# Optimization experiments

Hardware: AMD Instinct MI355X
Metric: run time of the kernel (lower is better)

## Reference

```python
import jax, jax.numpy as jnp
import numpy as np

GAMMA = 0.99
LAM = 0.95
CLIP = 0.2
VALUE_COEFF = 0.5
ENTROPY_COEFF = 0.01
T = 500_000
S = 128
A = 16


def _mlp(x, W1, b1, W2, b2, W3, b3):
    h = jax.nn.relu(x @ W1 + b1)
    h = jax.nn.relu(h @ W2 + b2)
    return h @ W3 + b3


def setup_inputs() -> dict:
    key = jax.random.key(0)
    ks = jax.random.split(key, 12)
    states = jax.random.normal(ks[0], (T, S), dtype=jnp.float32)
    next_states = jax.random.normal(ks[1], (T, S), dtype=jnp.float32)
    rewards = jax.random.normal(ks[2], (T,), dtype=jnp.float32)
    dones = (jax.random.uniform(ks[3], (T,)) < 0.01).astype(jnp.float32)
    actions = jax.random.randint(ks[4], (T,), 0, A)
    # old log-probs of taken actions (valid log-probabilities)
    old_logp = jnp.log(jax.random.uniform(ks[5], (T,), minval=1e-3, maxval=1.0))

    def lin(k, fan_in, fan_out):
        lim = 1.0 / np.sqrt(fan_in)
        return jax.random.uniform(k, (fan_in, fan_out), minval=-lim, maxval=lim, dtype=jnp.float32)

    return {
        'states': states, 'next_states': next_states, 'rewards': rewards,
        'dones': dones, 'actions': actions, 'old_logp': old_logp,
        'aW1': lin(ks[6], S, 64), 'ab1': jnp.zeros((64,), jnp.float32),
        'aW2': lin(ks[7], 64, 64), 'ab2': jnp.zeros((64,), jnp.float32),
        'aW3': lin(ks[8], 64, A), 'ab3': jnp.zeros((A,), jnp.float32),
        'cW1': lin(ks[9], S, 64), 'cb1': jnp.zeros((64,), jnp.float32),
        'cW2': lin(ks[10], 64, 64), 'cb2': jnp.zeros((64,), jnp.float32),
        'cW3': lin(ks[11], 64, 1), 'cb3': jnp.zeros((1,), jnp.float32),
    }


def reference(states, next_states, rewards, dones, actions, old_logp,
              aW1, ab1, aW2, ab2, aW3, ab3,
              cW1, cb1, cW2, cb2, cW3, cb3):
    # ---- critic values and TD deltas ----
    values = _mlp(states, cW1, cb1, cW2, cb2, cW3, cb3)[:, 0]        # [T]
    next_values = _mlp(next_states, cW1, cb1, cW2, cb2, cW3, cb3)[:, 0]
    not_done = 1.0 - dones
    deltas = rewards + GAMMA * next_values * not_done - values       # [T]

    # ---- GAE: reverse-time linear recurrence a_t = c_t * a_{t+1} + d_t ----
    coef = GAMMA * LAM * not_done

    def step(carry, cd):
        c, d = cd
        a = c * carry + d
        return a, a

    _, advantages = jax.lax.scan(step, jnp.float32(0.0), (coef, deltas), reverse=True)
    returns = advantages + values
    adv_n = (advantages - advantages.mean()) / (jnp.std(advantages, ddof=1) + 1e-8)

    # ---- actor: clipped surrogate ----
    probs = jax.nn.softmax(_mlp(states, aW1, ab1, aW2, ab2, aW3, ab3), axis=-1)  # [T, A]
    logp = jnp.log(jnp.take_along_axis(probs, actions[:, None], axis=1))[:, 0]   # [T]
    ratios = jnp.exp(logp - old_logp)
    surr1 = ratios * adv_n
    surr2 = jnp.clip(ratios, 1.0 - CLIP, 1.0 + CLIP) * adv_n
    actor_loss = -jnp.minimum(surr1, surr2).mean()

    # ---- critic MSE loss ----
    critic_loss = jnp.mean((values - returns) ** 2)

    # ---- entropy bonus ----
    entropy_loss = jnp.mean(-jnp.sum(probs * jnp.log(probs + 1e-8), axis=-1))

    total_loss = actor_loss + VALUE_COEFF * critic_loss - ENTROPY_COEFF * entropy_loss
    return jnp.stack([total_loss, actor_loss, critic_loss, entropy_loss])
```

## Files before the change

kernel.cpp:

```cpp
#include <hip/hip_runtime.h>
#include <hip/hip_bf16.h>

#define T_N 500000
#define NTILE 31250
#define NBLK 512
#define NWAVES (NBLK * 4)
#define NCHUNK 4096
#define CHUNKL 128
#define NPART 1024

typedef __attribute__((ext_vector_type(8))) short short8v;
typedef __attribute__((ext_vector_type(4))) float float4v;

__device__ __forceinline__ short f2bf(float f) {
    __hip_bfloat16 b = __float2bfloat16(f);
    return *reinterpret_cast<short*>(&b);
}

__device__ __forceinline__ short8v cvt8(const float4 a, const float4 b) {
    short8v r;
    r[0] = f2bf(a.x); r[1] = f2bf(a.y); r[2] = f2bf(a.z); r[3] = f2bf(a.w);
    r[4] = f2bf(b.x); r[5] = f2bf(b.y); r[6] = f2bf(b.z); r[7] = f2bf(b.w);
    return r;
}

#define FC1 0
#define FA1 16
#define FC2 32
#define FA2 40
#define FA3 48
#define NFRAG 50

__global__ __launch_bounds__(64) void k_pack(
    const float* __restrict__ cW1, const float* __restrict__ aW1,
    const float* __restrict__ cW2, const float* __restrict__ aW2,
    const float* __restrict__ aW3, short8v* __restrict__ packed)
{
    const int f = blockIdx.x, l = threadIdx.x;
    const int g = l >> 4, col = l & 15;
    const float* W; int s, c, ncol;
    if (f < FA1)      { W = cW1; s = f >> 2;         c = f & 3;         ncol = 64; }
    else if (f < FC2) { W = aW1; s = (f - FA1) >> 2; c = (f - FA1) & 3; ncol = 64; }
    else if (f < FA2) { W = cW2; s = (f - FC2) >> 2; c = (f - FC2) & 3; ncol = 64; }
    else if (f < FA3) { W = aW2; s = (f - FA2) >> 2; c = (f - FA2) & 3; ncol = 64; }
    else              { W = aW3; s = f - FA3;        c = 0;             ncol = 16; }
    short8v frag;
    #pragma unroll
    for (int j = 0; j < 8; ++j) {
        int k = s * 32 + g * 8 + j;
        frag[j] = f2bf(W[k * ncol + c * 16 + col]);
    }
    packed[f * 64 + l] = frag;
}

__device__ __forceinline__ void store_h(short (*hb)[68], const float4v* acc, int g, int q) {
    #pragma unroll
    for (int c = 0; c < 4; ++c)
        #pragma unroll
        for (int r = 0; r < 4; ++r)
            hb[g * 4 + r][c * 16 + q] = f2bf(fmaxf(acc[c][r], 0.f));
}

__global__ __launch_bounds__(256) void k_mlp(
    const float* __restrict__ states, const float* __restrict__ next_states,
    const float* __restrict__ rewards, const float* __restrict__ dones,
    const int* __restrict__ actions, const float* __restrict__ old_logp,
    const short8v* __restrict__ pk,
    const float* __restrict__ cb1, const float* __restrict__ ab1,
    const float* __restrict__ cb2, const float* __restrict__ ab2,
    const float* __restrict__ ab3,
    const float* __restrict__ cW3, const float* __restrict__ cb3,
    float* __restrict__ delta_o, float* __restrict__ coef_o,
    float* __restrict__ ratio_o, float* __restrict__ ent_o)
{
    __shared__ __align__(16) short8v spk[NFRAG * 64];
    __shared__ __align__(16) short hlds[4][2][16][68];
    const int wv = threadIdx.x >> 6, l = threadIdx.x & 63;
    const int g = l >> 4, q = l & 15;
    short (*h0)[68] = hlds[wv][0];
    short (*h1)[68] = hlds[wv][1];

    for (int i = threadIdx.x; i < NFRAG * 64; i += 256) spk[i] = pk[i];
    __syncthreads();

    int tile = blockIdx.x * 4 + wv;
    if (tile >= NTILE) return;

    float bc1[4], bc2[4], ba1[4], ba2[4], w3[4];
    #pragma unroll
    for (int c = 0; c < 4; ++c) {
        bc1[c] = cb1[c * 16 + q];
        bc2[c] = cb2[c * 16 + q];
        ba1[c] = ab1[c * 16 + q];
        ba2[c] = ab2[c * 16 + q];
        w3[c]  = cW3[c * 16 + q];
    }
    const float ab3q = ab3[q];
    const float cb3v = cb3[0];

    float4 rs[8], rn[8];
    {
        const float* xs = states + ((long long)tile * 16 + q) * 128 + g * 8;
        const float* xn = next_states + ((long long)tile * 16 + q) * 128 + g * 8;
        #pragma unroll
        for (int s = 0; s < 4; ++s) {
            rs[2 * s]     = *reinterpret_cast<const float4*>(xs + s * 32);
            rs[2 * s + 1] = *reinterpret_cast<const float4*>(xs + s * 32 + 4);
            rn[2 * s]     = *reinterpret_cast<const float4*>(xn + s * 32);
            rn[2 * s + 1] = *reinterpret_cast<const float4*>(xn + s * 32 + 4);
        }
    }

    while (true) {
        const int next = tile + NWAVES;
        const long long r0 = (long long)tile * 16;

        short8v sa[4], na[4];
        #pragma unroll
        for (int s = 0; s < 4; ++s) {
            sa[s] = cvt8(rs[2 * s], rs[2 * s + 1]);
            na[s] = cvt8(rn[2 * s], rn[2 * s + 1]);
        }

        if (next < NTILE) {
            const float* xs = states + ((long long)next * 16 + q) * 128 + g * 8;
            const float* xn = next_states + ((long long)next * 16 + q) * 128 + g * 8;
            #pragma unroll
            for (int s = 0; s < 4; ++s) {
                rs[2 * s]     = *reinterpret_cast<const float4*>(xs + s * 32);
                rs[2 * s + 1] = *reinterpret_cast<const float4*>(xs + s * 32 + 4);
                rn[2 * s]     = *reinterpret_cast<const float4*>(xn + s * 32);
                rn[2 * s + 1] = *reinterpret_cast<const float4*>(xn + s * 32 + 4);
            }
        }

        float4v accC[4], accN[4];
        #pragma unroll
        for (int c = 0; c < 4; ++c) {
            accC[c] = (float4v){bc1[c], bc1[c], bc1[c], bc1[c]};
            accN[c] = accC[c];
        }
        #pragma unroll
        for (int s = 0; s < 4; ++s) {
            #pragma unroll
            for (int c = 0; c < 4; ++c) {
                short8v w = spk[(FC1 + s * 4 + c) * 64 + l];
                accC[c] = __builtin_amdgcn_mfma_f32_16x16x32_bf16(sa[s], w, accC[c], 0, 0, 0);
                accN[c] = __builtin_amdgcn_mfma_f32_16x16x32_bf16(na[s], w, accN[c], 0, 0, 0);
            }
        }
        store_h(h0, accC, g, q);
        store_h(h1, accN, g, q);

        float4v c2C[4], c2N[4];
        #pragma unroll
        for (int c = 0; c < 4; ++c) {
            c2C[c] = (float4v){bc2[c], bc2[c], bc2[c], bc2[c]};
            c2N[c] = c2C[c];
        }
        #pragma unroll
        for (int s = 0; s < 2; ++s) {
            short8v aC = *reinterpret_cast<const short8v*>(&h0[q][s * 32 + g * 8]);
            short8v aN = *reinterpret_cast<const short8v*>(&h1[q][s * 32 + g * 8]);
            #pragma unroll
            for (int c = 0; c < 4; ++c) {
                short8v w = spk[(FC2 + s * 4 + c) * 64 + l];
                c2C[c] = __builtin_amdgcn_mfma_f32_16x16x32_bf16(aC, w, c2C[c], 0, 0, 0);
                c2N[c] = __builtin_amdgcn_mfma_f32_16x16x32_bf16(aN, w, c2N[c], 0, 0, 0);
            }
        }
        float vr[4] = {0.f, 0.f, 0.f, 0.f}, nr[4] = {0.f, 0.f, 0.f, 0.f};
        #pragma unroll
        for (int c = 0; c < 4; ++c) {
            #pragma unroll
            for (int r = 0; r < 4; ++r) {
                vr[r] = fmaf(fmaxf(c2C[c][r], 0.f), w3[c], vr[r]);
                nr[r] = fmaf(fmaxf(c2N[c][r], 0.f), w3[c], nr[r]);
            }
        }
        #pragma unroll
        for (int o = 1; o < 16; o <<= 1)
            #pragma unroll
            for (int r = 0; r < 4; ++r) {
                vr[r] += __shfl_xor(vr[r], o);
                nr[r] += __shfl_xor(nr[r], o);
            }
        float v[4], nv[4];
        #pragma unroll
        for (int r = 0; r < 4; ++r) { v[r] = vr[r] + cb3v; nv[r] = nr[r] + cb3v; }

        float4v aA[4];
        #pragma unroll
        for (int c = 0; c < 4; ++c) aA[c] = (float4v){ba1[c], ba1[c], ba1[c], ba1[c]};
        #pragma unroll
        for (int s = 0; s < 4; ++s)
            #pragma unroll
            for (int c = 0; c < 4; ++c)
                aA[c] = __builtin_amdgcn_mfma_f32_16x16x32_bf16(sa[s], spk[(FA1 + s * 4 + c) * 64 + l], aA[c], 0, 0, 0);
        store_h(h0, aA, g, q);

        float4v a2[4];
        #pragma unroll
        for (int c = 0; c < 4; ++c) a2[c] = (float4v){ba2[c], ba2[c], ba2[c], ba2[c]};
        #pragma unroll
        for (int s = 0; s < 2; ++s) {
            short8v aa = *reinterpret_cast<const short8v*>(&h0[q][s * 32 + g * 8]);
            #pragma unroll
            for (int c = 0; c < 4; ++c)
                a2[c] = __builtin_amdgcn_mfma_f32_16x16x32_bf16(aa, spk[(FA2 + s * 4 + c) * 64 + l], a2[c], 0, 0, 0);
        }
        store_h(h1, a2, g, q);

        float4v a3 = (float4v){ab3q, ab3q, ab3q, ab3q};
        #pragma unroll
        for (int s = 0; s < 2; ++s) {
            short8v aa = *reinterpret_cast<const short8v*>(&h1[q][s * 32 + g * 8]);
            a3 = __builtin_amdgcn_mfma_f32_16x16x32_bf16(aa, spk[(FA3 + s) * 64 + l], a3, 0, 0, 0);
        }

        float lg[4], mx[4], pe[4], se[4], tt[4], ent[4], logp[4];
        #pragma unroll
        for (int r = 0; r < 4; ++r) { lg[r] = a3[r]; mx[r] = lg[r]; }
        #pragma unroll
        for (int o = 1; o < 16; o <<= 1)
            #pragma unroll
            for (int r = 0; r < 4; ++r) mx[r] = fmaxf(mx[r], __shfl_xor(mx[r], o));
        #pragma unroll
        for (int r = 0; r < 4; ++r) {
            pe[r] = __expf(lg[r] - mx[r]);
            se[r] = pe[r];
            tt[r] = pe[r] * lg[r];
        }
        #pragma unroll
        for (int o = 1; o < 16; o <<= 1)
            #pragma unroll
            for (int r = 0; r < 4; ++r) {
                se[r] += __shfl_xor(se[r], o);
                tt[r] += __shfl_xor(tt[r], o);
            }
        const int4 av = *reinterpret_cast<const int4*>(&actions[r0 + g * 4]);
        const int act[4] = {av.x, av.y, av.z, av.w};
        #pragma unroll
        for (int r = 0; r < 4; ++r) {
            float ls = __logf(se[r]);
            ent[r] = mx[r] + ls - tt[r] / se[r];
            float sel = __shfl(lg[r], (l & 48) | act[r]);
            logp[r] = sel - mx[r] - ls;
        }

        if (q == 0) {
            const long long rb = r0 + g * 4;
            const float4 rw = *reinterpret_cast<const float4*>(&rewards[rb]);
            const float4 dn = *reinterpret_cast<const float4*>(&dones[rb]);
            const float4 ol = *reinterpret_cast<const float4*>(&old_logp[rb]);
            const float rwv[4] = {rw.x, rw.y, rw.z, rw.w};
            const float dnv[4] = {dn.x, dn.y, dn.z, dn.w};
            const float olv[4] = {ol.x, ol.y, ol.z, ol.w};
            const float GL = 0.99f * 0.95f;
            float dl[4], cf[4], rt[4];
            #pragma unroll
            for (int r = 0; r < 4; ++r) {
                float nd = 1.f - dnv[r];
                dl[r] = fmaf(0.99f * nd, nv[r], rwv[r]) - v[r];
                cf[r] = GL * nd;
                rt[r] = __expf(logp[r] - olv[r]);
            }
            float4 t;
            t.x = dl[0]; t.y = dl[1]; t.z = dl[2]; t.w = dl[3];
            *reinterpret_cast<float4*>(&delta_o[rb]) = t;
            t.x = cf[0]; t.y = cf[1]; t.z = cf[2]; t.w = cf[3];
            *reinterpret_cast<float4*>(&coef_o[rb]) = t;
            t.x = rt[0]; t.y = rt[1]; t.z = rt[2]; t.w = rt[3];
            *reinterpret_cast<float4*>(&ratio_o[rb]) = t;
            t.x = ent[0]; t.y = ent[1]; t.z = ent[2]; t.w = ent[3];
            *reinterpret_cast<float4*>(&ent_o[rb]) = t;
        }

        if (next >= NTILE) break;
        tile = next;
    }
}

__global__ __launch_bounds__(256) void k_gae_chunk(
    const float* __restrict__ coef, const float* __restrict__ delta,
    float* __restrict__ P, float* __restrict__ Q)
{
    const int c = blockIdx.x * 256 + threadIdx.x;
    const long long lo = (long long)c * CHUNKL;
    float p = 1.f, a = 0.f;
    if (lo < T_N) {
        const int n = (int)((T_N - lo < CHUNKL) ? (T_N - lo) : CHUNKL);
        for (int j = (n >> 2) - 1; j >= 0; --j) {
            float4 cfv = *reinterpret_cast<const float4*>(&coef[lo + 4 * j]);
            float4 dlv = *reinterpret_cast<const float4*>(&delta[lo + 4 * j]);
            a = fmaf(cfv.w, a, dlv.w);
            a = fmaf(cfv.z, a, dlv.z);
            a = fmaf(cfv.y, a, dlv.y);
            a = fmaf(cfv.x, a, dlv.x);
            p *= cfv.x * cfv.y * cfv.z * cfv.w;
        }
    }
    P[c] = p; Q[c] = a;
}

__global__ __launch_bounds__(1024) void k_gae_scan(
    const float* __restrict__ P, const float* __restrict__ Q,
    float* __restrict__ carry)
{
    __shared__ float sp[1024], sq[1024];
    const int t = threadIdx.x, b = t * 4;
    float p = P[b + 3], q = Q[b + 3];
    #pragma unroll
    for (int c = 2; c >= 0; --c) {
        float pc = P[b + c], qc = Q[b + c];
        q = fmaf(pc, q, qc);
        p = pc * p;
    }
    sp[t] = p; sq[t] = q;
    __syncthreads();
    for (int d = 1; d < 1024; d <<= 1) {
        float pp = sp[t], qq = sq[t];
        float p2 = 1.f, q2 = 0.f;
        const bool has = (t + d) < 1024;
        if (has) { p2 = sp[t + d]; q2 = sq[t + d]; }
        __syncthreads();
        if (has) { sp[t] = pp * p2; sq[t] = fmaf(pp, q2, qq); }
        __syncthreads();
    }
    float x = (t + 1 < 1024) ? sq[t + 1] : 0.f;
    #pragma unroll
    for (int c = 3; c >= 0; --c) {
        carry[b + c] = x;
        x = fmaf(P[b + c], x, Q[b + c]);
    }
}

__global__ __launch_bounds__(256) void k_gae_apply(
    const float* __restrict__ coef, const float* __restrict__ delta,
    const float* __restrict__ carry, float* __restrict__ adv,
    float* __restrict__ part)
{
    const int c = blockIdx.x * 256 + threadIdx.x;
    const long long lo = (long long)c * CHUNKL;
    float s = 0.f, s2 = 0.f;
    if (lo < T_N) {
        const int n = (int)((T_N - lo < CHUNKL) ? (T_N - lo) : CHUNKL);
        float a = carry[c];
        for (int j = (n >> 2) - 1; j >= 0; --j) {
            float4 cfv = *reinterpret_cast<const float4*>(&coef[lo + 4 * j]);
            float4 dlv = *reinterpret_cast<const float4*>(&delta[lo + 4 * j]);
            float a3 = fmaf(cfv.w, a, dlv.w);
            float a2v = fmaf(cfv.z, a3, dlv.z);
            float a1 = fmaf(cfv.y, a2v, dlv.y);
            float a0 = fmaf(cfv.x, a1, dlv.x);
            float4 o; o.x = a0; o.y = a1; o.z = a2v; o.w = a3;
            *reinterpret_cast<float4*>(&adv[lo + 4 * j]) = o;
            a = a0;
            s += a0 + a1 + a2v + a3;
            s2 += a0 * a0 + a1 * a1 + a2v * a2v + a3 * a3;
        }
    }
    #pragma unroll
    for (int o = 32; o > 0; o >>= 1) { s += __shfl_down(s, o); s2 += __shfl_down(s2, o); }
    __shared__ float l0[4], l1[4];
    const int wv = threadIdx.x >> 6, ln = threadIdx.x & 63;
    if (ln == 0) { l0[wv] = s; l1[wv] = s2; }
    __syncthreads();
    if (threadIdx.x == 0) {
        part[blockIdx.x * 2]     = l0[0] + l0[1] + l0[2] + l0[3];
        part[blockIdx.x * 2 + 1] = l1[0] + l1[1] + l1[2] + l1[3];
    }
}

__global__ __launch_bounds__(256) void k_actor(
    const float* __restrict__ adv, const float* __restrict__ ratio,
    const float* __restrict__ ent, const float* __restrict__ part,
    float* __restrict__ part4)
{
    __shared__ float st[2];
    if (threadIdx.x == 0) {
        float S = 0.f, S2 = 0.f;
        #pragma unroll
        for (int i = 0; i < 16; ++i) { S += part[2 * i]; S2 += part[2 * i + 1]; }
        const float Tf = (float)T_N;
        float mean = S / Tf;
        float var = (S2 - S * S / Tf) / (Tf - 1.f);
        st[0] = mean;
        st[1] = 1.f / (sqrtf(fmaxf(var, 0.f)) + 1e-8f);
    }
    __syncthreads();
    const float mean = st[0], isd = st[1];
    float sm = 0.f, se = 0.f;
    for (long long i = (long long)blockIdx.x * 256 + threadIdx.x; i < T_N;
         i += (long long)gridDim.x * 256) {
        float an = (adv[i] - mean) * isd;
        float rt = ratio[i];
        float s1 = rt * an;
        float s2v = fminf(fmaxf(rt, 0.8f), 1.2f) * an;
        sm += fminf(s1, s2v);
        se += ent[i];
    }
    #pragma unroll
    for (int o = 32; o > 0; o >>= 1) { sm += __shfl_down(sm, o); se += __shfl_down(se, o); }
    __shared__ float l0[4], l1[4];
    const int wv = threadIdx.x >> 6, ln = threadIdx.x & 63;
    if (ln == 0) { l0[wv] = sm; l1[wv] = se; }
    __syncthreads();
    if (threadIdx.x == 0) {
        part4[blockIdx.x * 2]     = l0[0] + l0[1] + l0[2] + l0[3];
        part4[blockIdx.x * 2 + 1] = l1[0] + l1[1] + l1[2] + l1[3];
    }
}

__global__ __launch_bounds__(1024) void k_final(
    const float* __restrict__ part4, const float* __restrict__ part,
    float* __restrict__ out)
{
    const int t = threadIdx.x;
    float sm = part4[t * 2], se = part4[t * 2 + 1];
    #pragma unroll
    for (int o = 32; o > 0; o >>= 1) { sm += __shfl_down(sm, o); se += __shfl_down(se, o); }
    __shared__ float l0[16], l1[16];
    const int wv = t >> 6, ln = t & 63;
    if (ln == 0) { l0[wv] = sm; l1[wv] = se; }
    __syncthreads();
    if (t == 0) {
        float SM = 0.f, SE = 0.f;
        #pragma unroll
        for (int i = 0; i < 16; ++i) { SM += l0[i]; SE += l1[i]; }
        float S2 = 0.f;
        #pragma unroll
        for (int i = 0; i < 16; ++i) S2 += part[2 * i + 1];
        const float Tf = (float)T_N;
        float actor_loss = -SM / Tf;
        float ent_loss = SE / Tf;
        float critic_loss = S2 / Tf;
        float total = actor_loss + 0.5f * critic_loss - 0.01f * ent_loss;
        out[0] = total; out[1] = actor_loss; out[2] = critic_loss; out[3] = ent_loss;
    }
}

extern "C" void kernel_launch(void* const* d_in, const int* in_sizes, int n_in,
                              void* d_out, int out_size, void* d_ws, size_t ws_size,
                              hipStream_t stream) {
    (void)in_sizes; (void)n_in; (void)out_size; (void)ws_size;
    const float* states      = (const float*)d_in[0];
    const float* next_states = (const float*)d_in[1];
    const float* rewards     = (const float*)d_in[2];
    const float* dones       = (const float*)d_in[3];
    const int*   actions     = (const int*)d_in[4];
    const float* old_logp    = (const float*)d_in[5];
    const float* aW1 = (const float*)d_in[6];  const float* ab1 = (const float*)d_in[7];
    const float* aW2 = (const float*)d_in[8];  const float* ab2 = (const float*)d_in[9];
    const float* aW3 = (const float*)d_in[10]; const float* ab3 = (const float*)d_in[11];
    const float* cW1 = (const float*)d_in[12]; const float* cb1 = (const float*)d_in[13];
    const float* cW2 = (const float*)d_in[14]; const float* cb2 = (const float*)d_in[15];
    const float* cW3 = (const float*)d_in[16]; const float* cb3 = (const float*)d_in[17];
    float* out = (float*)d_out;

    float* ws = (float*)d_ws;
    float* delta = ws;
    float* coef  = ws + 1 * (size_t)T_N;
    float* ratio = ws + 2 * (size_t)T_N;
    float* entb  = ws + 3 * (size_t)T_N;
    float* adv   = ws + 4 * (size_t)T_N;
    float* P     = ws + 5 * (size_t)T_N;
    float* Q     = P + NCHUNK;
    float* carry = Q + NCHUNK;
    float* part  = carry + NCHUNK;
    float* part4 = part + 32;
    short8v* packed = (short8v*)(part4 + 2048);

    k_pack<<<NFRAG, 64, 0, stream>>>(cW1, aW1, cW2, aW2, aW3, packed);
    k_mlp<<<NBLK, 256, 0, stream>>>(
        states, next_states, rewards, dones, actions, old_logp, packed,
        cb1, ab1, cb2, ab2, ab3, cW3, cb3, delta, coef, ratio, entb);
    k_gae_chunk<<<NCHUNK / 256, 256, 0, stream>>>(coef, delta, P, Q);
    k_gae_scan<<<1, 1024, 0, stream>>>(P, Q, carry);
    k_gae_apply<<<NCHUNK / 256, 256, 0, stream>>>(coef, delta, carry, adv, part);
    k_actor<<<NPART, 256, 0, stream>>>(adv, ratio, entb, part, part4);
    k_final<<<1, 1024, 0, stream>>>(part4, part, out);
}
```

Before: 211.8 us.

## Move softmax epilogue from MLP kernel into actor reduction, store bf16 logits

The MLP kernel no longer does the per-row softmax, entropy, log-prob and delta/coef computation. It now writes only the critic values, next values and the 16 actor logits per row, the logits as bf16. The GAE kernels recompute delta and coef on the fly from values, rewards and dones, and the actor kernel recomputes the softmax, entropy and ratio from the stored logits. The aim is to cut shuffle-heavy epilogue work and extra input loads from the MLP kernel, which dominates the runtime. The cost is more intermediate memory traffic (a 32-byte logit row instead of a few floats), four input streams in each GAE pass, and some precision loss from rounding logits to bf16.

```diff
diff --git a/kernel.cpp b/kernel.cpp
--- a/kernel.cpp
+++ b/kernel.cpp
@@ -15,6 +15,9 @@
 __device__ __forceinline__ short f2bf(float f) {
     __hip_bfloat16 b = __float2bfloat16(f);
     return *reinterpret_cast<short*>(&b);
+}
+__device__ __forceinline__ float bf2f(short s) {
+    return __uint_as_float(((unsigned)(unsigned short)s) << 16);
 }
 
 __device__ __forceinline__ short8v cvt8(const float4 a, const float4 b) {
@@ -63,15 +66,13 @@
 
 __global__ __launch_bounds__(256) void k_mlp(
     const float* __restrict__ states, const float* __restrict__ next_states,
-    const float* __restrict__ rewards, const float* __restrict__ dones,
-    const int* __restrict__ actions, const float* __restrict__ old_logp,
     const short8v* __restrict__ pk,
     const float* __restrict__ cb1, const float* __restrict__ ab1,
     const float* __restrict__ cb2, const float* __restrict__ ab2,
     const float* __restrict__ ab3,
     const float* __restrict__ cW3, const float* __restrict__ cb3,
-    float* __restrict__ delta_o, float* __restrict__ coef_o,
-    float* __restrict__ ratio_o, float* __restrict__ ent_o)
+    float* __restrict__ v_o, float* __restrict__ nv_o,
+    short* __restrict__ logit_o)
 {
     __shared__ __align__(16) short8v spk[NFRAG * 64];
     __shared__ __align__(16) short hlds[4][2][16][68];
@@ -185,9 +186,13 @@
                 vr[r] += __shfl_xor(vr[r], o);
                 nr[r] += __shfl_xor(nr[r], o);
             }
-        float v[4], nv[4];
-        #pragma unroll
-        for (int r = 0; r < 4; ++r) { v[r] = vr[r] + cb3v; nv[r] = nr[r] + cb3v; }
+        if (q == 0) {
+            float4 tv, tn;
+            tv.x = vr[0] + cb3v; tv.y = vr[1] + cb3v; tv.z = vr[2] + cb3v; tv.w = vr[3] + cb3v;
+            tn.x = nr[0] + cb3v; tn.y = nr[1] + cb3v; tn.z = nr[2] + cb3v; tn.w = nr[3] + cb3v;
+            *reinterpret_cast<float4*>(&v_o[r0 + g * 4])  = tv;
+            *reinterpret_cast<float4*>(&nv_o[r0 + g * 4]) = tn;
+        }
 
         float4v aA[4];
         #pragma unroll
@@ -217,72 +222,25 @@
             short8v aa = *reinterpret_cast<const short8v*>(&h1[q][s * 32 + g * 8]);
             a3 = __builtin_amdgcn_mfma_f32_16x16x32_bf16(aa, spk[(FA3 + s) * 64 + l], a3, 0, 0, 0);
         }
-
-        float lg[4], mx[4], pe[4], se[4], tt[4], ent[4], logp[4];
-        #pragma unroll
-        for (int r = 0; r < 4; ++r) { lg[r] = a3[r]; mx[r] = lg[r]; }
-        #pragma unroll
-        for (int o = 1; o < 16; o <<= 1)
-            #pragma unroll
-            for (int r = 0; r < 4; ++r) mx[r] = fmaxf(mx[r], __shfl_xor(mx[r], o));
-        #pragma unroll
-        for (int r = 0; r < 4; ++r) {
-            pe[r] = __expf(lg[r] - mx[r]);
-            se[r] = pe[r];
-            tt[r] = pe[r] * lg[r];
-        }
-        #pragma unroll
-        for (int o = 1; o < 16; o <<= 1)
-            #pragma unroll
-            for (int r = 0; r < 4; ++r) {
-                se[r] += __shfl_xor(se[r], o);
-                tt[r] += __shfl_xor(tt[r], o);
-            }
-        const int4 av = *reinterpret_cast<const int4*>(&actions[r0 + g * 4]);
-        const int act[4] = {av.x, av.y, av.z, av.w};
-        #pragma unroll
-        for (int r = 0; r < 4; ++r) {
-            float ls = __logf(se[r]);
-            ent[r] = mx[r] + ls - tt[r] / se[r];
-            float sel = __shfl(lg[r], (l & 48) | act[r]);
-            logp[r] = sel - mx[r] - ls;
-        }
-
-        if (q == 0) {
-            const long long rb = r0 + g * 4;
-            const float4 rw = *reinterpret_cast<const float4*>(&rewards[rb]);
-            const float4 dn = *reinterpret_cast<const float4*>(&dones[rb]);
-            const float4 ol = *reinterpret_cast<const float4*>(&old_logp[rb]);
-            const float rwv[4] = {rw.x, rw.y, rw.z, rw.w};
-            const float dnv[4] = {dn.x, dn.y, dn.z, dn.w};
-            const float olv[4] = {ol.x, ol.y, ol.z, ol.w};
-            const float GL = 0.99f * 0.95f;
-            float dl[4], cf[4], rt[4];
-            #pragma unroll
-            for (int r = 0; r < 4; ++r) {
-                float nd = 1.f - dnv[r];
-                dl[r] = fmaf(0.99f * nd, nv[r], rwv[r]) - v[r];
-                cf[r] = GL * nd;
-                rt[r] = __expf(logp[r] - olv[r]);
-            }
-            float4 t;
-            t.x = dl[0]; t.y = dl[1]; t.z = dl[2]; t.w = dl[3];
-            *reinterpret_cast<float4*>(&delta_o[rb]) = t;
-            t.x = cf[0]; t.y = cf[1]; t.z = cf[2]; t.w = cf[3];
-            *reinterpret_cast<float4*>(&coef_o[rb]) = t;
-            t.x = rt[0]; t.y = rt[1]; t.z = rt[2]; t.w = rt[3];
-            *reinterpret_cast<float4*>(&ratio_o[rb]) = t;
-            t.x = ent[0]; t.y = ent[1]; t.z = ent[2]; t.w = ent[3];
-            *reinterpret_cast<float4*>(&ent_o[rb]) = t;
-        }
+        #pragma unroll
+        for (int r = 0; r < 4; ++r)
+            logit_o[(r0 + g * 4 + r) * 16 + q] = f2bf(a3[r]);
 
         if (next >= NTILE) break;
         tile = next;
     }
 }
 
+__device__ __forceinline__ void dc_elem(float v, float nv, float rw, float dn,
+                                        float& d, float& c) {
+    float nd = 1.f - dn;
+    d = fmaf(0.99f * nd, nv, rw) - v;
+    c = (0.99f * 0.95f) * nd;
+}
+
 __global__ __launch_bounds__(256) void k_gae_chunk(
-    const float* __restrict__ coef, const float* __restrict__ delta,
+    const float* __restrict__ v_i, const float* __restrict__ nv_i,
+    const float* __restrict__ rewards, const float* __restrict__ dones,
     float* __restrict__ P, float* __restrict__ Q)
 {
     const int c = blockIdx.x * 256 + threadIdx.x;
@@ -291,13 +249,20 @@
     if (lo < T_N) {
         const int n = (int)((T_N - lo < CHUNKL) ? (T_N - lo) : CHUNKL);
         for (int j = (n >> 2) - 1; j >= 0; --j) {
-            float4 cfv = *reinterpret_cast<const float4*>(&coef[lo + 4 * j]);
-            float4 dlv = *reinterpret_cast<const float4*>(&delta[lo + 4 * j]);
-            a = fmaf(cfv.w, a, dlv.w);
-            a = fmaf(cfv.z, a, dlv.z);
-            a = fmaf(cfv.y, a, dlv.y);
-            a = fmaf(cfv.x, a, dlv.x);
-            p *= cfv.x * cfv.y * cfv.z * cfv.w;
+            float4 vv = *reinterpret_cast<const float4*>(&v_i[lo + 4 * j]);
+            float4 nn = *reinterpret_cast<const float4*>(&nv_i[lo + 4 * j]);
+            float4 rw = *reinterpret_cast<const float4*>(&rewards[lo + 4 * j]);
+            float4 dn = *reinterpret_cast<const float4*>(&dones[lo + 4 * j]);
+            float d0, c0, d1, c1, d2, c2, d3, c3;
+            dc_elem(vv.x, nn.x, rw.x, dn.x, d0, c0);
+            dc_elem(vv.y, nn.y, rw.y, dn.y, d1, c1);
+            dc_elem(vv.z, nn.z, rw.z, dn.z, d2, c2);
+            dc_elem(vv.w, nn.w, rw.w, dn.w, d3, c3);
+            a = fmaf(c3, a, d3);
+            a = fmaf(c2, a, d2);
+            a = fmaf(c1, a, d1);
+            a = fmaf(c0, a, d0);
+            p *= c0 * c1 * c2 * c3;
         }
     }
     P[c] = p; Q[c] = a;
@@ -336,7 +301,8 @@
 }
 
 __global__ __launch_bounds__(256) void k_gae_apply(
-    const float* __restrict__ coef, const float* __restrict__ delta,
+    const float* __restrict__ v_i, const float* __restrict__ nv_i,
+    const float* __restrict__ rewards, const float* __restrict__ dones,
     const float* __restrict__ carry, float* __restrict__ adv,
     float* __restrict__ part)
 {
@@ -347,12 +313,19 @@
         const int n = (int)((T_N - lo < CHUNKL) ? (T_N - lo) : CHUNKL);
         float a = carry[c];
         for (int j = (n >> 2) - 1; j >= 0; --j) {
-            float4 cfv = *reinterpret_cast<const float4*>(&coef[lo + 4 * j]);
-            float4 dlv = *reinterpret_cast<const float4*>(&delta[lo + 4 * j]);
-            float a3 = fmaf(cfv.w, a, dlv.w);
-            float a2v = fmaf(cfv.z, a3, dlv.z);
-            float a1 = fmaf(cfv.y, a2v, dlv.y);
-            float a0 = fmaf(cfv.x, a1, dlv.x);
+            float4 vv = *reinterpret_cast<const float4*>(&v_i[lo + 4 * j]);
+            float4 nn = *reinterpret_cast<const float4*>(&nv_i[lo + 4 * j]);
+            float4 rw = *reinterpret_cast<const float4*>(&rewards[lo + 4 * j]);
+            float4 dn = *reinterpret_cast<const float4*>(&dones[lo + 4 * j]);
+            float d0, c0, d1, c1, d2, c2, d3, c3;
+            dc_elem(vv.x, nn.x, rw.x, dn.x, d0, c0);
+            dc_elem(vv.y, nn.y, rw.y, dn.y, d1, c1);
+            dc_elem(vv.z, nn.z, rw.z, dn.z, d2, c2);
+            dc_elem(vv.w, nn.w, rw.w, dn.w, d3, c3);
+            float a3 = fmaf(c3, a, d3);
+            float a2v = fmaf(c2, a3, d2);
+            float a1 = fmaf(c1, a2v, d1);
+            float a0 = fmaf(c0, a1, d0);
             float4 o; o.x = a0; o.y = a1; o.z = a2v; o.w = a3;
             *reinterpret_cast<float4*>(&adv[lo + 4 * j]) = o;
             a = a0;
@@ -373,9 +346,9 @@
 }
 
 __global__ __launch_bounds__(256) void k_actor(
-    const float* __restrict__ adv, const float* __restrict__ ratio,
-    const float* __restrict__ ent, const float* __restrict__ part,
-    float* __restrict__ part4)
+    const float* __restrict__ adv, const short* __restrict__ logits,
+    const float* __restrict__ old_logp, const int* __restrict__ actions,
+    const float* __restrict__ part, float* __restrict__ part4)
 {
     __shared__ float st[2];
     if (threadIdx.x == 0) {
@@ -390,21 +363,41 @@
     }
     __syncthreads();
     const float mean = st[0], isd = st[1];
-    float sm = 0.f, se = 0.f;
+    float sm = 0.f, sent = 0.f;
     for (long long i = (long long)blockIdx.x * 256 + threadIdx.x; i < T_N;
          i += (long long)gridDim.x * 256) {
+        const short8v* lp = reinterpret_cast<const short8v*>(logits) + i * 2;
+        short8v lo0 = lp[0], lo1 = lp[1];
+        float lg[16];
+        #pragma unroll
+        for (int j = 0; j < 8; ++j) { lg[j] = bf2f(lo0[j]); lg[8 + j] = bf2f(lo1[j]); }
+        float m = lg[0];
+        #pragma unroll
+        for (int a = 1; a < 16; ++a) m = fmaxf(m, lg[a]);
+        float se = 0.f, tt = 0.f;
+        #pragma unroll
+        for (int a = 0; a < 16; ++a) {
+            float e = __expf(lg[a] - m);
+            se += e;
+            tt = fmaf(e, lg[a], tt);
+        }
+        float ls = __logf(se);
+        float ent = m + ls - tt / se;
+        const int act = actions[i];
+        float lsel = lg[0];
+        #pragma unroll
+        for (int a = 1; a < 16; ++a) lsel = (a == act) ? lg[a] : lsel;
+        float logp = lsel - m - ls;
+        float rt = __expf(logp - old_logp[i]);
         float an = (adv[i] - mean) * isd;
-        float rt = ratio[i];
-        float s1 = rt * an;
-        float s2v = fminf(fmaxf(rt, 0.8f), 1.2f) * an;
-        sm += fminf(s1, s2v);
-        se += ent[i];
-    }
-    #pragma unroll
-    for (int o = 32; o > 0; o >>= 1) { sm += __shfl_down(sm, o); se += __shfl_down(se, o); }
+        sm += fminf(rt * an, fminf(fmaxf(rt, 0.8f), 1.2f) * an);
+        sent += ent;
+    }
+    #pragma unroll
+    for (int o = 32; o > 0; o >>= 1) { sm += __shfl_down(sm, o); sent += __shfl_down(sent, o); }
     __shared__ float l0[4], l1[4];
     const int wv = threadIdx.x >> 6, ln = threadIdx.x & 63;
-    if (ln == 0) { l0[wv] = sm; l1[wv] = se; }
+    if (ln == 0) { l0[wv] = sm; l1[wv] = sent; }
     __syncthreads();
     if (threadIdx.x == 0) {
         part4[blockIdx.x * 2]     = l0[0] + l0[1] + l0[2] + l0[3];
@@ -458,13 +451,12 @@
     const float* cW3 = (const float*)d_in[16]; const float* cb3 = (const float*)d_in[17];
     float* out = (float*)d_out;
 
-    float* ws = (float*)d_ws;
-    float* delta = ws;
-    float* coef  = ws + 1 * (size_t)T_N;
-    float* ratio = ws + 2 * (size_t)T_N;
-    float* entb  = ws + 3 * (size_t)T_N;
-    float* adv   = ws + 4 * (size_t)T_N;
-    float* P     = ws + 5 * (size_t)T_N;
+    short* logits = (short*)d_ws;
+    float* fbase = (float*)(logits + (size_t)T_N * 16);
+    float* v_ws  = fbase;
+    float* nv_ws = fbase + (size_t)T_N;
+    float* adv   = fbase + 2 * (size_t)T_N;
+    float* P     = fbase + 3 * (size_t)T_N;
     float* Q     = P + NCHUNK;
     float* carry = Q + NCHUNK;
     float* part  = carry + NCHUNK;
@@ -473,11 +465,11 @@
 
     k_pack<<<NFRAG, 64, 0, stream>>>(cW1, aW1, cW2, aW2, aW3, packed);
     k_mlp<<<NBLK, 256, 0, stream>>>(
-        states, next_states, rewards, dones, actions, old_logp, packed,
-        cb1, ab1, cb2, ab2, ab3, cW3, cb3, delta, coef, ratio, entb);
-    k_gae_chunk<<<NCHUNK / 256, 256, 0, stream>>>(coef, delta, P, Q);
+        states, next_states, packed,
+        cb1, ab1, cb2, ab2, ab3, cW3, cb3, v_ws, nv_ws, logits);
+    k_gae_chunk<<<NCHUNK / 256, 256, 0, stream>>>(v_ws, nv_ws, rewards, dones, P, Q);
     k_gae_scan<<<1, 1024, 0, stream>>>(P, Q, carry);
-    k_gae_apply<<<NCHUNK / 256, 256, 0, stream>>>(coef, delta, carry, adv, part);
-    k_actor<<<NPART, 256, 0, stream>>>(adv, ratio, entb, part, part4);
+    k_gae_apply<<<NCHUNK / 256, 256, 0, stream>>>(v_ws, nv_ws, rewards, dones, carry, adv, part);
+    k_actor<<<NPART, 256, 0, stream>>>(adv, logits, old_logp, actions, part, part4);
     k_final<<<1, 1024, 0, stream>>>(part4, part, out);
 }
```

Result: no change. 209.2 us (-1.2%).
